# Kernel tuning notes

Hardware: AMD Instinct MI355X
Metric: run time of the kernel (lower is better)

## Reference

```python
import jax, jax.numpy as jnp
import numpy as np

NUM_CLASSES = 10
BASE_TEMPERATURE = 0.07
TEMP = 0.1


def setup_inputs() -> dict:
    key = jax.random.key(0)
    k1, k2 = jax.random.split(key)
    features = jax.random.normal(k1, (8192, 128), dtype=jnp.float32)
    targets = jax.random.randint(k2, (8192,), 0, NUM_CLASSES, dtype=jnp.int64)
    return {"features": features, "targets": targets}


def reference(features, targets):
    bs = features.shape[0]
    dtype = features.dtype
    # one-hot label matrix -> positive mask via label agreement
    one_hot = jax.nn.one_hot(targets, NUM_CLASSES, dtype=dtype)          # [bs, C]
    mask_pos_full = one_hot @ one_hot.T                                  # [bs, bs], 1 if same class
    mask_negatives = jnp.ones((bs, bs), dtype=dtype) - mask_pos_full
    mask_positives = mask_pos_full - jnp.eye(bs, dtype=dtype)            # exclude self
    logits_mask = mask_positives + mask_negatives                        # == 1 - eye
    # pairwise similarity logits
    logits = (features @ features.T) / TEMP                              # [bs, bs]
    logits_max = jax.lax.stop_gradient(jnp.max(logits, axis=1, keepdims=True))
    logits = logits - logits_max
    exp_logits = jnp.exp(logits) * logits_mask
    log_prob = logits - jnp.log(jnp.sum(exp_logits, axis=1, keepdims=True) + 1e-20)
    mean_log_prob_pos = jnp.sum(mask_positives * log_prob, axis=1) / (
        jnp.sum(mask_positives, axis=1) + 1e-20
    )
    loss = -(TEMP / BASE_TEMPERATURE) * jnp.mean(mean_log_prob_pos)
    avg_pos = jnp.mean(jnp.sum(mask_positives, axis=1))
    avg_neg = jnp.mean(jnp.sum(mask_negatives, axis=1))
    return (loss, avg_pos, avg_neg)
```

## Files before the change

kernel.cpp:

```cpp
#include <hip/hip_runtime.h>

#define N 8192
#define KD 128
#define NCLS 10
#define NCH 8
#define CHUNK (N / NCH)

typedef __attribute__((ext_vector_type(4))) int intx4;


__global__ __launch_bounds__(256) void k_conv(const float* __restrict__ F,
                                              const int* __restrict__ tgt,
                                              float* __restrict__ diag10,
                                              int* __restrict__ Q,
                                              float* __restrict__ S,
                                              int* __restrict__ cnt,
                                              float* __restrict__ PS) {
    int t = threadIdx.x;
    if (blockIdx.x < 64) {
        int b = blockIdx.x;
        int row0 = b * 128;
        int k = t & 127, h = t >> 7;
        __shared__ int lh[NCLS];
        if (t < NCLS) lh[t] = 0;
        __syncthreads();
        if (t < 128) atomicAdd(&lh[tgt[row0 + t]], 1);
        float local[NCLS];
#pragma unroll
        for (int c = 0; c < NCLS; ++c) local[c] = 0.f;
        for (int ii = 0; ii < 64; ++ii) {
            int row = row0 + h * 64 + ii;
            float v = F[(size_t)row * KD + k];
            int c = tgt[row];
#pragma unroll
            for (int cc = 0; cc < NCLS; ++cc) local[cc] += (cc == c) ? v : 0.f;
        }
        __shared__ float red[2][NCLS][KD];
#pragma unroll
        for (int cc = 0; cc < NCLS; ++cc) red[h][cc][k] = local[cc];
        __syncthreads();
        if (h == 0) {
#pragma unroll
            for (int cc = 0; cc < NCLS; ++cc)
                atomicAdd(&S[cc * KD + k], red[0][cc][k] + red[1][cc][k]);
            if (t < NCLS) atomicAdd(&cnt[t], lh[t]);
        }
    } else {
        int row0 = (blockIdx.x - 64) * 16;
        if (t < 16) PS[row0 + t] = 0.f;
        int col4 = t & 31;
        int rg = t >> 5;
#pragma unroll
        for (int sw = 0; sw < 2; ++sw) {
            int row = row0 + sw * 8 + rg;
            float4 v = *(const float4*)(F + (size_t)row * KD + col4 * 4);
            float sq = v.x * v.x + v.y * v.y + v.z * v.z + v.w * v.w;
#pragma unroll
            for (int off = 16; off >= 1; off >>= 1) sq += __shfl_xor(sq, off);
            if (col4 == 0) diag10[row] = 10.f * sq;
            int q0 = __float2int_rn(30.f * fminf(fmaxf(v.x, -4.2f), 4.2f));
            int q1 = __float2int_rn(30.f * fminf(fmaxf(v.y, -4.2f), 4.2f));
            int q2 = __float2int_rn(30.f * fminf(fmaxf(v.z, -4.2f), 4.2f));
            int q3 = __float2int_rn(30.f * fminf(fmaxf(v.w, -4.2f), 4.2f));
            int dq = (q0 & 255) | ((q1 & 255) << 8) | ((q2 & 255) << 16) | ((q3 & 255) << 24);
            int idx = (row >> 4) * 512 + (col4 >> 4) * 256 + ((col4 >> 2) & 3) * 64 +
                      (row & 15) * 4 + (col4 & 3);
            Q[idx] = dq;
        }
    }
}

__global__ __launch_bounds__(256, 2) void k_pair(const unsigned char* __restrict__ Qb,
                                                 const float* __restrict__ diag10,
                                                 float* __restrict__ PS) {
    int bx = blockIdx.x, ch = blockIdx.y;
    int tid = threadIdx.x;
    int w = tid >> 6, lane = tid & 63;
    int quad = lane >> 4, l16 = lane & 15;
    int row0 = bx * 64;

    float d = diag10[row0 + lane];
#pragma unroll
    for (int off = 32; off >= 1; off >>= 1) d = fminf(d, __shfl_xor(d, off));
    int thrq = (int)((d - 60.f) * 90.f);

    intx4 af[4][2];
#pragma unroll
    for (int it = 0; it < 4; ++it)
#pragma unroll
        for (int ks = 0; ks < 2; ++ks)
            af[it][ks] = *(const intx4*)(Qb + (size_t)(bx * 4 + it) * 2048 + ks * 1024 + lane * 16);

    intx4 bufs[2][4][2];
    {
        int col0 = ch * CHUNK + w * 64;
        const unsigned char* bp = Qb + (size_t)(col0 >> 4) * 2048 + lane * 16;
#pragma unroll
        for (int tj = 0; tj < 4; ++tj)
#pragma unroll
            for (int ks = 0; ks < 2; ++ks)
                bufs[0][tj][ks] = *(const intx4*)(bp + tj * 2048 + ks * 1024);
    }

#pragma unroll
    for (int s = 0; s < 8; ++s) {
        if (s < 7) {
            int sn = s + 1;
            int coln = (ch + (sn >> 2) * 4) * CHUNK + ((sn & 3) * 4 + w) * 64;
            const unsigned char* bp = Qb + (size_t)(coln >> 4) * 2048 + lane * 16;
#pragma unroll
            for (int tj = 0; tj < 4; ++tj)
#pragma unroll
                for (int ks = 0; ks < 2; ++ks)
                    bufs[(s + 1) & 1][tj][ks] = *(const intx4*)(bp + tj * 2048 + ks * 1024);
        }

        int col0 = (ch + (s >> 2) * 4) * CHUNK + ((s & 3) * 4 + w) * 64;

        intx4 acc[4][4];
#pragma unroll
        for (int it = 0; it < 4; ++it)
#pragma unroll
            for (int tj = 0; tj < 4; ++tj)
                acc[it][tj] = (intx4){0, 0, 0, 0};

#pragma unroll
        for (int ks = 0; ks < 2; ++ks)
#pragma unroll
            for (int it = 0; it < 4; ++it)
#pragma unroll
                for (int tj = 0; tj < 4; ++tj)
                    acc[it][tj] = __builtin_amdgcn_mfma_i32_16x16x64_i8(
                        af[it][ks], bufs[s & 1][tj][ks], acc[it][tj], 0, 0, 0);

        int mx = -2147483647;
#pragma unroll
        for (int it = 0; it < 4; ++it)
#pragma unroll
            for (int tj = 0; tj < 4; ++tj) {
                int a01 = max(acc[it][tj][0], acc[it][tj][1]);
                int a23 = max(acc[it][tj][2], acc[it][tj][3]);
                mx = max(mx, max(a01, a23));
            }

        if (__any(mx > thrq)) {
#pragma unroll
            for (int it = 0; it < 4; ++it)
#pragma unroll
                for (int r = 0; r < 4; ++r) {
                    int grow = row0 + it * 16 + quad * 4 + r;
                    float Mrow = diag10[grow];
                    float rs = 0.f;
#pragma unroll
                    for (int tj = 0; tj < 4; ++tj) {
                        int gcol = col0 + tj * 16 + l16;
                        float lv = (float)acc[it][tj][r] * (1.f / 90.f);
                        float ev = __expf(lv - Mrow);
                        rs += (grow == gcol) ? 0.f : ev;
                    }
                    rs += __shfl_xor(rs, 1, 16);
                    rs += __shfl_xor(rs, 2, 16);
                    rs += __shfl_xor(rs, 4, 16);
                    rs += __shfl_xor(rs, 8, 16);
                    if (l16 == 0) atomicAdd(&PS[grow], rs);
                }
        }
    }
}

__global__ __launch_bounds__(256) void k_final(const float* __restrict__ F,
                                               const int* __restrict__ tgt,
                                               const float* __restrict__ diag10,
                                               const float* __restrict__ PS,
                                               const float* __restrict__ S,
                                               int* __restrict__ cnt,
                                               float* __restrict__ acc,
                                               float* __restrict__ out) {
    __shared__ float Ss[NCLS * KD];
    __shared__ int cs[NCLS];
    int t = threadIdx.x;
    for (int i = t; i < NCLS * KD; i += 256) Ss[i] = S[i];
    if (t < NCLS) cs[t] = cnt[t];
    __syncthreads();

    int g = t >> 2, q = t & 3;
    int row = blockIdx.x * 64 + g;
    int c = tgt[row];
    float dot = 0.f;
#pragma unroll
    for (int i = 0; i < 8; ++i) {
        float4 f = *(const float4*)(F + (size_t)row * KD + i * 16 + q * 4);
        float4 s = *(const float4*)(Ss + c * KD + i * 16 + q * 4);
        dot += f.x * s.x + f.y * s.y + f.z * s.z + f.w * s.w;
    }
    dot += __shfl_xor(dot, 1, 4);
    dot += __shfl_xor(dot, 2, 4);

    float mlp = 0.f;
    if (q == 0) {
        float M = diag10[row];
        float pp = 10.f * dot - M;
        float T = PS[row];
        float np = (float)(cs[c] - 1);
        mlp = (np < 0.5f) ? 0.f : (pp - np * (M + __logf(T + 1e-20f))) / np;
    }
#pragma unroll
    for (int off = 32; off >= 1; off >>= 1) mlp += __shfl_xor(mlp, off);
    __shared__ float wsum[4];
    int lane = t & 63, w = t >> 6;
    if (lane == 0) wsum[w] = mlp;
    __syncthreads();
    if (t == 0) {
        atomicAdd(acc, (wsum[0] + wsum[1]) + (wsum[2] + wsum[3]));
        __threadfence();
        int old = atomicAdd(&cnt[12], 1);
        if (old == (int)gridDim.x - 1) {
            float tot = atomicAdd(acc, 0.0f);
            double sp = 0.0, sn = 0.0;
            for (int cc = 0; cc < NCLS; ++cc) {
                double n = (double)cs[cc];
                sp += n * (n - 1.0);
                sn += n * ((double)N - n);
            }
            out[0] = (float)(-(0.1 / 0.07) * ((double)tot / (double)N));
            out[1] = (float)(sp / (double)N);
            out[2] = (float)(sn / (double)N);
        }
    }
}

extern "C" void kernel_launch(void* const* d_in, const int* in_sizes, int n_in,
                              void* d_out, int out_size, void* d_ws, size_t ws_size,
                              hipStream_t stream) {
    const float* F = (const float*)d_in[0];
    const int* tgt = (const int*)d_in[1];
    float* out = (float*)d_out;
    char* ws = (char*)d_ws;

    int* cnt = (int*)(ws);
    float* acc = (float*)(ws + 64);
    float* S = (float*)(ws + 128);
    float* PS = (float*)(ws + 8192);
    float* diag10 = (float*)(ws + 65536);
    int* Q = (int*)(ws + (1u << 20));

    hipMemsetAsync(ws, 0, 8192, stream);
    k_conv<<<576, 256, 0, stream>>>(F, tgt, diag10, Q, S, cnt, PS);
    k_pair<<<dim3(N / 64, NCH / 2), 256, 0, stream>>>((const unsigned char*)Q, diag10, PS);
    k_final<<<N / 64, 256, 0, stream>>>(F, tgt, diag10, PS, S, cnt, acc, out);
}
```

Before: 90.25 us.

## Exploit Gram matrix symmetry to halve pairwise int8 MFMA tiles

Each block now covers only half of the column tiles, using a cyclic offset so every unordered tile pair is computed once. Each tile's exponentials are summed both along rows and along columns, so the transposed contribution is added to the column rows' partition sums. A global minimum of the diagonal is taken with an atomicMin in k_conv and used as the skip threshold, replacing the per-block minimum. This roughly halves the MFMA and load work, but adds an extra column-reduction pass of exp and atomics per tile, plus uneven extra work for the blocks that handle the antipodal tiles.

```diff
diff --git a/kernel.cpp b/kernel.cpp
--- a/kernel.cpp
+++ b/kernel.cpp
@@ -3,8 +3,6 @@
 #define N 8192
 #define KD 128
 #define NCLS 10
-#define NCH 8
-#define CHUNK (N / NCH)
 
 typedef __attribute__((ext_vector_type(4))) int intx4;
 
@@ -15,7 +13,8 @@
                                               int* __restrict__ Q,
                                               float* __restrict__ S,
                                               int* __restrict__ cnt,
-                                              float* __restrict__ PS) {
+                                              float* __restrict__ PS,
+                                              int* __restrict__ Gi) {
     int t = threadIdx.x;
     if (blockIdx.x < 64) {
         int b = blockIdx.x;
@@ -57,7 +56,11 @@
             float sq = v.x * v.x + v.y * v.y + v.z * v.z + v.w * v.w;
 #pragma unroll
             for (int off = 16; off >= 1; off >>= 1) sq += __shfl_xor(sq, off);
-            if (col4 == 0) diag10[row] = 10.f * sq;
+            if (col4 == 0) {
+                float dg = 10.f * sq;
+                diag10[row] = dg;
+                atomicMin(Gi, __float_as_int(dg));
+            }
             int q0 = __float2int_rn(30.f * fminf(fmaxf(v.x, -4.2f), 4.2f));
             int q1 = __float2int_rn(30.f * fminf(fmaxf(v.y, -4.2f), 4.2f));
             int q2 = __float2int_rn(30.f * fminf(fmaxf(v.z, -4.2f), 4.2f));
@@ -72,17 +75,15 @@
 
 __global__ __launch_bounds__(256, 2) void k_pair(const unsigned char* __restrict__ Qb,
                                                  const float* __restrict__ diag10,
-                                                 float* __restrict__ PS) {
-    int bx = blockIdx.x, ch = blockIdx.y;
+                                                 float* __restrict__ PS,
+                                                 const int* __restrict__ Gi) {
+    int bx = blockIdx.x, y = blockIdx.y;
     int tid = threadIdx.x;
     int w = tid >> 6, lane = tid & 63;
     int quad = lane >> 4, l16 = lane & 15;
     int row0 = bx * 64;
 
-    float d = diag10[row0 + lane];
-#pragma unroll
-    for (int off = 32; off >= 1; off >>= 1) d = fminf(d, __shfl_xor(d, off));
-    int thrq = (int)((d - 60.f) * 90.f);
+    int thrq = (int)((__int_as_float(*Gi) - 60.f) * 90.f);
 
     intx4 af[4][2];
 #pragma unroll
@@ -91,9 +92,11 @@
         for (int ks = 0; ks < 2; ++ks)
             af[it][ks] = *(const intx4*)(Qb + (size_t)(bx * 4 + it) * 2048 + ks * 1024 + lane * 16);
 
+    bool ext = (y == 0) && (bx < 64) && (w == 0);
+
     intx4 bufs[2][4][2];
     {
-        int col0 = ch * CHUNK + w * 64;
+        int col0 = ((bx + y * 16 + w) & 127) * 64;
         const unsigned char* bp = Qb + (size_t)(col0 >> 4) * 2048 + lane * 16;
 #pragma unroll
         for (int tj = 0; tj < 4; ++tj)
@@ -103,19 +106,26 @@
     }
 
 #pragma unroll
-    for (int s = 0; s < 8; ++s) {
-        if (s < 7) {
-            int sn = s + 1;
-            int coln = (ch + (sn >> 2) * 4) * CHUNK + ((sn & 3) * 4 + w) * 64;
+    for (int s = 0; s < 4; ++s) {
+        if (s < 3) {
+            int coln = ((bx + y * 16 + (s + 1) * 4 + w) & 127) * 64;
             const unsigned char* bp = Qb + (size_t)(coln >> 4) * 2048 + lane * 16;
 #pragma unroll
             for (int tj = 0; tj < 4; ++tj)
 #pragma unroll
                 for (int ks = 0; ks < 2; ++ks)
                     bufs[(s + 1) & 1][tj][ks] = *(const intx4*)(bp + tj * 2048 + ks * 1024);
-        }
-
-        int col0 = (ch + (s >> 2) * 4) * CHUNK + ((s & 3) * 4 + w) * 64;
+        } else if (ext) {
+            int coln = (bx + 64) * 64;
+            const unsigned char* bp = Qb + (size_t)(coln >> 4) * 2048 + lane * 16;
+#pragma unroll
+            for (int tj = 0; tj < 4; ++tj)
+#pragma unroll
+                for (int ks = 0; ks < 2; ++ks)
+                    bufs[0][tj][ks] = *(const intx4*)(bp + tj * 2048 + ks * 1024);
+        }
+
+        int col0 = ((bx + y * 16 + s * 4 + w) & 127) * 64;
 
         intx4 acc[4][4];
 #pragma unroll
@@ -123,7 +133,6 @@
 #pragma unroll
             for (int tj = 0; tj < 4; ++tj)
                 acc[it][tj] = (intx4){0, 0, 0, 0};
-
 #pragma unroll
         for (int ks = 0; ks < 2; ++ks)
 #pragma unroll
@@ -144,6 +153,7 @@
             }
 
         if (__any(mx > thrq)) {
+            bool has_diag = (col0 == row0);
 #pragma unroll
             for (int it = 0; it < 4; ++it)
 #pragma unroll
@@ -164,6 +174,84 @@
                     rs += __shfl_xor(rs, 8, 16);
                     if (l16 == 0) atomicAdd(&PS[grow], rs);
                 }
+            if (!has_diag) {
+#pragma unroll
+                for (int tj = 0; tj < 4; ++tj) {
+                    int gcol = col0 + tj * 16 + l16;
+                    float Mcol = diag10[gcol];
+                    float cs_ = 0.f;
+#pragma unroll
+                    for (int it = 0; it < 4; ++it)
+#pragma unroll
+                        for (int r = 0; r < 4; ++r)
+                            cs_ += __expf((float)acc[it][tj][r] * (1.f / 90.f) - Mcol);
+                    cs_ += __shfl_xor(cs_, 16);
+                    cs_ += __shfl_xor(cs_, 32);
+                    if (quad == 0) atomicAdd(&PS[gcol], cs_);
+                }
+            }
+        }
+    }
+
+    if (ext) {
+        int col0 = (bx + 64) * 64;
+        intx4 acc[4][4];
+#pragma unroll
+        for (int it = 0; it < 4; ++it)
+#pragma unroll
+            for (int tj = 0; tj < 4; ++tj)
+                acc[it][tj] = (intx4){0, 0, 0, 0};
+#pragma unroll
+        for (int ks = 0; ks < 2; ++ks)
+#pragma unroll
+            for (int it = 0; it < 4; ++it)
+#pragma unroll
+                for (int tj = 0; tj < 4; ++tj)
+                    acc[it][tj] = __builtin_amdgcn_mfma_i32_16x16x64_i8(
+                        af[it][ks], bufs[0][tj][ks], acc[it][tj], 0, 0, 0);
+
+        int mx = -2147483647;
+#pragma unroll
+        for (int it = 0; it < 4; ++it)
+#pragma unroll
+            for (int tj = 0; tj < 4; ++tj) {
+                int a01 = max(acc[it][tj][0], acc[it][tj][1]);
+                int a23 = max(acc[it][tj][2], acc[it][tj][3]);
+                mx = max(mx, max(a01, a23));
+            }
+        if (__any(mx > thrq)) {
+#pragma unroll
+            for (int it = 0; it < 4; ++it)
+#pragma unroll
+                for (int r = 0; r < 4; ++r) {
+                    int grow = row0 + it * 16 + quad * 4 + r;
+                    float Mrow = diag10[grow];
+                    float rs = 0.f;
+#pragma unroll
+                    for (int tj = 0; tj < 4; ++tj) {
+                        float lv = (float)acc[it][tj][r] * (1.f / 90.f);
+                        rs += __expf(lv - Mrow);
+                    }
+                    rs += __shfl_xor(rs, 1, 16);
+                    rs += __shfl_xor(rs, 2, 16);
+                    rs += __shfl_xor(rs, 4, 16);
+                    rs += __shfl_xor(rs, 8, 16);
+                    if (l16 == 0) atomicAdd(&PS[grow], rs);
+                }
+#pragma unroll
+            for (int tj = 0; tj < 4; ++tj) {
+                int gcol = col0 + tj * 16 + l16;
+                float Mcol = diag10[gcol];
+                float cs_ = 0.f;
+#pragma unroll
+                for (int it = 0; it < 4; ++it)
+#pragma unroll
+                    for (int r = 0; r < 4; ++r)
+                        cs_ += __expf((float)acc[it][tj][r] * (1.f / 90.f) - Mcol);
+                cs_ += __shfl_xor(cs_, 16);
+                cs_ += __shfl_xor(cs_, 32);
+                if (quad == 0) atomicAdd(&PS[gcol], cs_);
+            }
         }
     }
 }
@@ -241,11 +329,13 @@
     float* acc = (float*)(ws + 64);
     float* S = (float*)(ws + 128);
     float* PS = (float*)(ws + 8192);
+    int* Gi = (int*)(ws + 49152);
     float* diag10 = (float*)(ws + 65536);
     int* Q = (int*)(ws + (1u << 20));
 
     hipMemsetAsync(ws, 0, 8192, stream);
-    k_conv<<<576, 256, 0, stream>>>(F, tgt, diag10, Q, S, cnt, PS);
-    k_pair<<<dim3(N / 64, NCH / 2), 256, 0, stream>>>((const unsigned char*)Q, diag10, PS);
+    hipMemsetAsync(ws + 49152, 0x7F, 4, stream);
+    k_conv<<<576, 256, 0, stream>>>(F, tgt, diag10, Q, S, cnt, PS, Gi);
+    k_pair<<<dim3(128, 4), 256, 0, stream>>>((const unsigned char*)Q, diag10, PS, Gi);
     k_final<<<N / 64, 256, 0, stream>>>(F, tgt, diag10, PS, S, cnt, acc, out);
 }
```

Measured after the change: 133.2 us. 1.48x slower.
